# Optimization experiments

Hardware: AMD Instinct MI355X
Metric: run time of the kernel (lower is better)

Reference implementation:

```python
import jax, jax.numpy as jnp
import numpy as np

B, S, HID = 2, 2048, 2048
N_HEADS, N_KV = 16, 8
HEAD_DIM = HID // N_HEADS  # 128
N_REP = N_HEADS // N_KV


def setup_inputs() -> dict:
    key = jax.random.key(0)
    ks = jax.random.split(key, 5)
    x = jax.random.normal(ks[0], (B, S, HID), dtype=jnp.float32)
    Wq = jax.random.normal(ks[1], (HID, N_HEADS * HEAD_DIM), dtype=jnp.float32) * 0.02
    Wk = jax.random.normal(ks[2], (HID, N_KV * HEAD_DIM), dtype=jnp.float32) * 0.02
    Wv = jax.random.normal(ks[3], (HID, N_KV * HEAD_DIM), dtype=jnp.float32) * 0.02
    Wo = jax.random.normal(ks[4], (N_HEADS * HEAD_DIM, HID), dtype=jnp.float32) * 0.02
    # standard RoPE frequencies: theta_i = 10000^(-2i/head_dim), angle = pos * theta_i
    inv_freq = 1.0 / (10000.0 ** (jnp.arange(0, HEAD_DIM, 2, dtype=jnp.float32) / HEAD_DIM))
    angles = jnp.arange(S, dtype=jnp.float32)[:, None] * inv_freq[None, :]  # [S, HEAD_DIM/2]
    return {
        "x": x, "Wq": Wq, "Wk": Wk, "Wv": Wv, "Wo": Wo,
        "freqs_cos": jnp.cos(angles), "freqs_sin": jnp.sin(angles),
        "start_pos": 0,
    }


def _rope(t, cos, sin):
    # t: [B, S, h, head_dim]; complex-view pairs are (even, odd) along last dim
    tr = t.reshape(*t.shape[:-1], -1, 2)
    re, im = tr[..., 0], tr[..., 1]
    cos = cos[None, :, None, :]
    sin = sin[None, :, None, :]
    out_re = re * cos - im * sin
    out_im = re * sin + im * cos
    return jnp.stack([out_re, out_im], axis=-1).reshape(t.shape)


def reference(x, Wq, Wk, Wv, Wo, freqs_cos, freqs_sin, start_pos):
    b, s, _ = x.shape
    xq = (x @ Wq).reshape(b, s, N_HEADS, HEAD_DIM)
    xk = (x @ Wk).reshape(b, s, N_KV, HEAD_DIM)
    xv = (x @ Wv).reshape(b, s, N_KV, HEAD_DIM)
    xq = _rope(xq, freqs_cos, freqs_sin)
    xk = _rope(xk, freqs_cos, freqs_sin)
    # repeat_kv: each kv head duplicated n_rep times consecutively
    xk = jnp.repeat(xk, N_REP, axis=2)  # [b, s, N_HEADS, hd]
    xv = jnp.repeat(xv, N_REP, axis=2)
    scale = 1.0 / jnp.sqrt(jnp.float32(HEAD_DIM))
    attn = jnp.einsum("bqhd,bkhd->bhqk", xq, xk) * scale
    attn = jax.nn.softmax(attn, axis=-1)
    out = jnp.einsum("bhqk,bkhd->bqhd", attn, xv).reshape(b, s, N_HEADS * HEAD_DIM)
    return out @ Wo
```

## Files before the change

kernel.cpp:

```cpp
#include <hip/hip_runtime.h>
#include <stdint.h>

#define DI __device__ __forceinline__

typedef unsigned short u16;
typedef unsigned int   u32;
typedef __attribute__((ext_vector_type(8))) short short8;
typedef __attribute__((ext_vector_type(4))) float f32x4;


DI u16 f2bf(float f) {
    u32 u = __float_as_uint(f);
    u32 r = u + 0x7fff + ((u >> 16) & 1);
    return (u16)(r >> 16);
}
DI u32 pk2bf(float a, float b) {
    return (u32)f2bf(a) | ((u32)f2bf(b) << 16);
}
DI float bf2f(u16 h) { return __uint_as_float(((u32)h) << 16); }

DI f32x4 mfma16(short8 a, short8 b, f32x4 c) {
    return __builtin_amdgcn_mfma_f32_16x16x32_bf16(a, b, c, 0, 0, 0);
}

DI void gload_lds16(const void* g, void* l) {
    __builtin_amdgcn_global_load_lds(
        (const __attribute__((address_space(1))) void*)g,
        (__attribute__((address_space(3))) void*)l, 16, 0, 0);
}

__global__ __launch_bounds__(256) void cvt_x(const float* __restrict__ x,
                                             u16* __restrict__ o, int n4) {
    int i = blockIdx.x * 256 + threadIdx.x;
    if (i >= n4) return;
    float4 v = *(const float4*)(x + (size_t)i * 4);
    uint2 p; p.x = pk2bf(v.x, v.y); p.y = pk2bf(v.z, v.w);
    *(uint2*)(o + (size_t)i * 4) = p;
}

__global__ __launch_bounds__(256) void transpose_cvt(const float* __restrict__ W,
                                                     u16* __restrict__ WT,
                                                     int K, int N) {
    __shared__ u16 tl[64][65];
    int tx = threadIdx.x & 15, ty = threadIdx.x >> 4;
    int tc = blockIdx.x * 64, tr = blockIdx.y * 64;
#pragma unroll
    for (int i = 0; i < 4; i++) {
        int r = tr + ty + i * 16;
        float4 v = *(const float4*)&W[(size_t)r * N + tc + tx * 4];
        tl[tx*4+0][ty+i*16] = f2bf(v.x);
        tl[tx*4+1][ty+i*16] = f2bf(v.y);
        tl[tx*4+2][ty+i*16] = f2bf(v.z);
        tl[tx*4+3][ty+i*16] = f2bf(v.w);
    }
    __syncthreads();
#pragma unroll
    for (int i = 0; i < 4; i++) {
        int n = tc + ty + i * 16;
        uint2 p;
        p.x = (u32)tl[ty+i*16][tx*4+0] | ((u32)tl[ty+i*16][tx*4+1] << 16);
        p.y = (u32)tl[ty+i*16][tx*4+2] | ((u32)tl[ty+i*16][tx*4+3] << 16);
        *(uint2*)&WT[(size_t)n * K + tr + tx * 4] = p;
    }
}

__global__ __launch_bounds__(256) void rope_kernel(u16* __restrict__ buf,
                                                   const float* __restrict__ fc,
                                                   const float* __restrict__ fs,
                                                   int H, int tokshift, int total,
                                                   float oscale) {
    int idx = blockIdx.x * 256 + threadIdx.x;
    if (idx >= total) return;
    int tok = idx >> tokshift;
    int rem = idx & ((1 << tokshift) - 1);
    int h = rem >> 6, j = rem & 63;
    int s = tok & 2047;
    size_t a = ((size_t)tok * H + h) * 128 + 2 * j;
    u32 v = *(u32*)(buf + a);
    float re = bf2f((u16)(v & 0xffff));
    float im = bf2f((u16)(v >> 16));
    float c = fc[s * 64 + j], sn = fs[s * 64 + j];
    *(u32*)(buf + a) = pk2bf((re * c - im * sn) * oscale,
                             (re * sn + im * c) * oscale);
}

__global__ __launch_bounds__(512) void gemm_qkv8(const u16* __restrict__ A,
                                                 const u16* __restrict__ BT,
                                                 u16* __restrict__ Qo,
                                                 u16* __restrict__ Ko,
                                                 u16* __restrict__ Vo) {
    __shared__ __align__(16) u16 SM[65536];
    char* smb = (char*)SM;
    const int tid = threadIdx.x;
    const int w = tid >> 6, l = tid & 63;
    const int l15 = l & 15, lh = l >> 4;
    const int wr = w >> 2, wc = w & 3;

    const int bid = blockIdx.x;
    const int sw = (bid & 7) * 32 + (bid >> 3);
    const int bx = sw & 15, by = sw >> 4;

    const char* Ag = (const char*)A  + (size_t)(by * 256) * 4096;
    const char* Bg = (const char*)BT + (size_t)(bx * 256) * 4096;

    const int r0 = tid >> 3;
    const int c0 = ((tid & 7) << 4) ^ (((tid >> 5) & 1) << 5);
    const int wb = w << 10;

#define STG_A(tt, bb, hh) do {                                              \
        const char* s_ = Ag + (size_t)((hh) * 128 + r0) * 4096 + (tt) * 128 + c0; \
        char* d_ = smb + (bb) * 65536 + (hh) * 16384 + wb;                  \
        gload_lds16(s_, d_);                                                \
        gload_lds16(s_ + (size_t)64 * 4096, d_ + 8192);                     \
    } while (0)
#define STG_B(tt, bb, hh) do {                                              \
        const char* s_ = Bg + (size_t)((hh) * 128 + r0) * 4096 + (tt) * 128 + c0; \
        char* d_ = smb + (bb) * 65536 + 32768 + (hh) * 16384 + wb;          \
        gload_lds16(s_, d_);                                                \
        gload_lds16(s_ + (size_t)64 * 4096, d_ + 8192);                     \
    } while (0)

    const int aoff = l15 * 128 + ((lh * 16) ^ (((l15 >> 2) & 1) << 5));

    const f32x4 fz = {0.f, 0.f, 0.f, 0.f};
    f32x4 acc[8][4];
#pragma unroll
    for (int m = 0; m < 8; m++)
#pragma unroll
        for (int n = 0; n < 4; n++) acc[m][n] = fz;

    STG_A(0, 0, 0); STG_A(0, 0, 1); STG_B(0, 0, 0); STG_B(0, 0, 1);
    STG_A(1, 1, 0);
    asm volatile("s_waitcnt vmcnt(2)" ::: "memory");
    __builtin_amdgcn_s_barrier();

    for (int t = 0; t < 32; ++t) {
        const int cur = t & 1;
        const int t1 = t + 1 < 32 ? t + 1 : 31;
        const int t2 = t + 2 < 32 ? t + 2 : 31;
        const char* Ab = smb + cur * 65536 + wr * 16384 + aoff;
        const char* Bb = smb + cur * 65536 + 32768 + (wc >> 1) * 16384
                         + (wc & 1) * 8192 + aoff;
        short8 aF[4][2], bF[4][2];

        STG_A(t1, cur ^ 1, 1);
#pragma unroll
        for (int m = 0; m < 4; m++) {
            aF[m][0] = *(const short8*)(Ab + m * 2048);
            aF[m][1] = *(const short8*)(Ab + m * 2048 + 64);
        }
#pragma unroll
        for (int n = 0; n < 2; n++) {
            bF[n][0] = *(const short8*)(Bb + n * 2048);
            bF[n][1] = *(const short8*)(Bb + n * 2048 + 64);
        }
        __builtin_amdgcn_s_setprio(1);
#pragma unroll
        for (int m = 0; m < 4; m++)
#pragma unroll
            for (int n = 0; n < 2; n++) {
                acc[m][n] = mfma16(aF[m][0], bF[n][0], acc[m][n]);
                acc[m][n] = mfma16(aF[m][1], bF[n][1], acc[m][n]);
            }
        __builtin_amdgcn_s_setprio(0);
        __builtin_amdgcn_s_barrier();

        STG_B(t1, cur ^ 1, 0);
#pragma unroll
        for (int n = 2; n < 4; n++) {
            bF[n][0] = *(const short8*)(Bb + n * 2048);
            bF[n][1] = *(const short8*)(Bb + n * 2048 + 64);
        }
        __builtin_amdgcn_s_setprio(1);
#pragma unroll
        for (int m = 0; m < 4; m++)
#pragma unroll
            for (int n = 2; n < 4; n++) {
                acc[m][n] = mfma16(aF[m][0], bF[n][0], acc[m][n]);
                acc[m][n] = mfma16(aF[m][1], bF[n][1], acc[m][n]);
            }
        __builtin_amdgcn_s_setprio(0);
        __builtin_amdgcn_s_barrier();

        STG_B(t1, cur ^ 1, 1);
#pragma unroll
        for (int m = 0; m < 4; m++) {
            aF[m][0] = *(const short8*)(Ab + (m + 4) * 2048);
            aF[m][1] = *(const short8*)(Ab + (m + 4) * 2048 + 64);
        }
        __builtin_amdgcn_s_setprio(1);
#pragma unroll
        for (int m = 0; m < 4; m++)
#pragma unroll
            for (int n = 0; n < 2; n++) {
                acc[m + 4][n] = mfma16(aF[m][0], bF[n][0], acc[m + 4][n]);
                acc[m + 4][n] = mfma16(aF[m][1], bF[n][1], acc[m + 4][n]);
            }
        __builtin_amdgcn_s_setprio(0);
        __builtin_amdgcn_s_barrier();

        STG_A(t2, cur, 0);
        __builtin_amdgcn_s_setprio(1);
#pragma unroll
        for (int m = 0; m < 4; m++)
#pragma unroll
            for (int n = 2; n < 4; n++) {
                acc[m + 4][n] = mfma16(aF[m][0], bF[n][0], acc[m + 4][n]);
                acc[m + 4][n] = mfma16(aF[m][1], bF[n][1], acc[m + 4][n]);
            }
        __builtin_amdgcn_s_setprio(0);
        asm volatile("s_waitcnt vmcnt(2)" ::: "memory");
        __builtin_amdgcn_s_barrier();
    }
#undef STG_A
#undef STG_B

    const int rbase = by * 256 + wr * 128 + lh * 4;
    const int cbase = bx * 256 + wc * 64 + l15;
    if (bx < 8) {
#pragma unroll
        for (int m = 0; m < 8; m++)
#pragma unroll
            for (int j = 0; j < 4; j++) {
                size_t ro = (size_t)(rbase + m * 16 + j) * 2048 + cbase;
#pragma unroll
                for (int n = 0; n < 4; n++)
                    Qo[ro + n * 16] = f2bf(acc[m][n][j]);
            }
    } else if (bx < 12) {
        const int ck = cbase - 2048;
#pragma unroll
        for (int m = 0; m < 8; m++)
#pragma unroll
            for (int j = 0; j < 4; j++) {
                size_t ro = (size_t)(rbase + m * 16 + j) * 1024 + ck;
#pragma unroll
                for (int n = 0; n < 4; n++)
                    Ko[ro + n * 16] = f2bf(acc[m][n][j]);
            }
    } else {
#pragma unroll
        for (int m = 0; m < 8; m++)
#pragma unroll
            for (int n = 0; n < 4; n++) {
                int tok = rbase + m * 16;
                int c = cbase + n * 16 - 3072;
                int bb2 = tok >> 11, ss = tok & 2047;
                int h2 = c >> 7, d = c & 127;
                uint2 v;
                v.x = pk2bf(acc[m][n][0], acc[m][n][1]);
                v.y = pk2bf(acc[m][n][2], acc[m][n][3]);
                *(uint2*)(Vo + (size_t)((bb2 * 8 + h2) * 128 + d) * 2048 + ss) = v;
            }
    }
}

__global__ __launch_bounds__(256) void gemm_wo(const u16* __restrict__ A,
                                               const u16* __restrict__ BT,
                                               float* __restrict__ Of,
                                               int M, int N, int K) {
    __shared__ u16 As[128 * 32];
    __shared__ u16 Bs[128 * 32];
    const int tid = threadIdx.x;
    const int w = tid >> 6, l = tid & 63;
    const int m0 = blockIdx.y * 128, n0 = blockIdx.x * 128;
    const int wr = w >> 1, wc = w & 1;
    const int l15 = l & 15, lh = l >> 4;

    const f32x4 fz = {0.f, 0.f, 0.f, 0.f};
    f32x4 acc[4][4];
#pragma unroll
    for (int m = 0; m < 4; m++)
#pragma unroll
        for (int n = 0; n < 4; n++) acc[m][n] = fz;

    const int rowA = w * 32 + (l >> 2);
    const int colb = (l & 3) * 8;

    for (int k0 = 0; k0 < K; k0 += 32) {
        __syncthreads();
#pragma unroll
        for (int c = 0; c < 2; c++) {
            gload_lds16(A  + (size_t)(m0 + rowA + c * 16) * K + k0 + colb,
                        &As[w * 1024 + c * 512]);
            gload_lds16(BT + (size_t)(n0 + rowA + c * 16) * K + k0 + colb,
                        &Bs[w * 1024 + c * 512]);
        }
        __syncthreads();
        short8 af[4], bfr[4];
#pragma unroll
        for (int m = 0; m < 4; m++)
            af[m] = *(const short8*)&As[(wr * 64 + m * 16 + l15) * 32 + lh * 8];
#pragma unroll
        for (int n = 0; n < 4; n++)
            bfr[n] = *(const short8*)&Bs[(wc * 64 + n * 16 + l15) * 32 + lh * 8];
#pragma unroll
        for (int m = 0; m < 4; m++)
#pragma unroll
            for (int n = 0; n < 4; n++)
                acc[m][n] = mfma16(af[m], bfr[n], acc[m][n]);
    }

    const int rbase = m0 + wr * 64 + lh * 4;
    const int cbase = n0 + wc * 64 + l15;
#pragma unroll
    for (int m = 0; m < 4; m++)
#pragma unroll
        for (int j = 0; j < 4; j++) {
            size_t ro = (size_t)(rbase + m * 16 + j) * N + cbase;
#pragma unroll
            for (int n = 0; n < 4; n++)
                Of[ro + n * 16] = acc[m][n][j];
        }
}

__global__ __launch_bounds__(512, 4) void attn_kernel(const u16* __restrict__ Q,
                                                      const u16* __restrict__ Kg,
                                                      const u16* __restrict__ Vg,
                                                      u16* __restrict__ O) {
    __shared__ __align__(16) u16 Ks[2][8192];
    __shared__ __align__(16) u16 Vs[2][8192];
    __shared__ __align__(16) u16 Ps[8][1024];
    const int tid = threadIdx.x;
    const int w = tid >> 6, l = tid & 63;
    const int qt = blockIdx.x, bh = blockIdx.y;
    const int b = bh >> 4, h = bh & 15, h2 = h >> 1;
    const int l15 = l & 15, lh = l >> 4;

    char* KsB = (char*)&Ks[0][0];
    char* VsB = (char*)&Vs[0][0];
    char* PsB = (char*)&Ps[w][0];

    const char* Kbase = (const char*)Kg + (size_t)b * 2048 * 2048 + h2 * 256;
    const char* Vbase = (const char*)Vg + (size_t)(b * 8 + h2) * 128 * 4096;
    const int X0 = tid * 16, X1 = 8192 + tid * 16;
    const int kr0 = X0 >> 8, kc0 = (X0 & 255) ^ ((kr0 & 7) << 4);
    const int kr1 = X1 >> 8, kc1 = (X1 & 255) ^ ((kr1 & 7) << 4);
    const int vd0 = X0 >> 7, vc0 = (X0 & 127) ^ ((vd0 & 7) << 4);
    const int vd1 = X1 >> 7, vc1 = (X1 & 127) ^ ((vd1 & 7) << 4);
    const int wb = w << 10;

#define STAGE(t, pb) do {                                              \
        const char* Kt = Kbase + (size_t)(t) * 131072;                 \
        const char* Vt = Vbase + (t) * 128;                            \
        char* kd = KsB + (pb) * 16384;                                 \
        char* vd = VsB + (pb) * 16384;                                 \
        gload_lds16(Kt + kr0 * 2048 + kc0, kd + wb);                   \
        gload_lds16(Kt + kr1 * 2048 + kc1, kd + 8192 + wb);            \
        gload_lds16(Vt + vd0 * 4096 + vc0, vd + wb);                   \
        gload_lds16(Vt + vd1 * 4096 + vc1, vd + 8192 + wb);            \
    } while (0)

    short8 qf[4];
    {
        const u16* qp = Q + ((size_t)(b * 2048 + qt * 128 + w * 16 + l15)) * 2048
                          + h * 128 + lh * 8;
#pragma unroll
        for (int ks = 0; ks < 4; ks++) qf[ks] = *(const short8*)(qp + ks * 32);
    }

    const f32x4 fz = {0.f, 0.f, 0.f, 0.f};
    f32x4 o[8];
#pragma unroll
    for (int n = 0; n < 8; n++) o[n] = fz;
    float mrow[4] = {-1e30f, -1e30f, -1e30f, -1e30f};
    float lsum[4] = {0.f, 0.f, 0.f, 0.f};

    STAGE(0, 0);

    for (int t = 0; t < 32; t++) {
        __syncthreads();
        const int pb = t & 1;
        if (t < 31) STAGE(t + 1, pb ^ 1);
        const char* kc = KsB + pb * 16384;
        const char* vc = VsB + pb * 16384;
        const int swz = (l15 & 7) << 4;

        f32x4 s[4];
#pragma unroll
        for (int ct = 0; ct < 4; ct++) {
            s[ct] = fz;
#pragma unroll
            for (int ks = 0; ks < 4; ks++) {
                short8 kf = *(const short8*)(kc + ((ct * 16 + l15) << 8)
                                                + ((ks * 64 + lh * 16) ^ swz));
                s[ct] = mfma16(qf[ks], kf, s[ct]);
            }
        }

        float pl[4];
#pragma unroll
        for (int r = 0; r < 4; r++)
            pl[r] = fmaxf(fmaxf(s[0][r], s[1][r]), fmaxf(s[2][r], s[3][r]));
        bool grow = (pl[0] > mrow[0] + 8.f) || (pl[1] > mrow[1] + 8.f) ||
                    (pl[2] > mrow[2] + 8.f) || (pl[3] > mrow[3] + 8.f);
        if (__any(grow)) {
#pragma unroll
            for (int r = 0; r < 4; r++) {
                float mx = pl[r];
                mx = fmaxf(mx, __shfl_xor(mx, 1));
                mx = fmaxf(mx, __shfl_xor(mx, 2));
                mx = fmaxf(mx, __shfl_xor(mx, 4));
                mx = fmaxf(mx, __shfl_xor(mx, 8));
                float mnew = fmaxf(mrow[r], mx);
                float fsc = exp2f(mrow[r] - mnew);
                mrow[r] = mnew;
                lsum[r] *= fsc;
#pragma unroll
                for (int n = 0; n < 8; n++) o[n][r] *= fsc;
            }
        }
#pragma unroll
        for (int r = 0; r < 4; r++) {
            float p0 = exp2f(s[0][r] - mrow[r]);
            float p1 = exp2f(s[1][r] - mrow[r]);
            float p2 = exp2f(s[2][r] - mrow[r]);
            float p3 = exp2f(s[3][r] - mrow[r]);
            lsum[r] += (p0 + p1) + (p2 + p3);
            const int rw = lh * 4 + r;
            const int rb = rw << 7;
            const int sw2 = (rw & 7) << 4;
            const int cb2 = l15 << 1;
            *(u16*)(PsB + (rb + (( 0 + cb2) ^ sw2))) =
                (u16)((__float_as_uint(p0) + 0x8000u) >> 16);
            *(u16*)(PsB + (rb + ((32 + cb2) ^ sw2))) =
                (u16)((__float_as_uint(p1) + 0x8000u) >> 16);
            *(u16*)(PsB + (rb + ((64 + cb2) ^ sw2))) =
                (u16)((__float_as_uint(p2) + 0x8000u) >> 16);
            *(u16*)(PsB + (rb + ((96 + cb2) ^ sw2))) =
                (u16)((__float_as_uint(p3) + 0x8000u) >> 16);
        }

#pragma unroll
        for (int ks2 = 0; ks2 < 2; ks2++) {
            short8 pf = *(const short8*)(PsB + ((l15 << 7)
                                + ((ks2 * 64 + lh * 16) ^ swz)));
#pragma unroll
            for (int n = 0; n < 8; n++) {
                short8 vf = *(const short8*)(vc + (((n * 16 + l15) << 7)
                                                  + ((ks2 * 64 + lh * 16) ^ swz)));
                o[n] = mfma16(pf, vf, o[n]);
            }
        }
    }

    const size_t ob = ((size_t)(b * 2048 + qt * 128 + w * 16 + lh * 4)) * 2048
                      + h * 128 + l15;
#pragma unroll
    for (int r = 0; r < 4; r++) {
        float ls = lsum[r];
        ls += __shfl_xor(ls, 1);
        ls += __shfl_xor(ls, 2);
        ls += __shfl_xor(ls, 4);
        ls += __shfl_xor(ls, 8);
        float li = 1.0f / ls;
#pragma unroll
        for (int n = 0; n < 8; n++)
            O[ob + (size_t)r * 2048 + n * 16] = f2bf(o[n][r] * li);
    }
#undef STAGE
}

extern "C" void kernel_launch(void* const* d_in, const int* in_sizes, int n_in,
                              void* d_out, int out_size, void* d_ws, size_t ws_size,
                              hipStream_t stream) {
    const float* x  = (const float*)d_in[0];
    const float* Wq = (const float*)d_in[1];
    const float* Wk = (const float*)d_in[2];
    const float* Wv = (const float*)d_in[3];
    const float* Wo = (const float*)d_in[4];
    const float* fc = (const float*)d_in[5];
    const float* fs = (const float*)d_in[6];
    float* out = (float*)d_out;

    uint8_t* ws = (uint8_t*)d_ws;
    u16* xb   = (u16*)(ws + 0);
    u16* wqkv = (u16*)(ws + 16777216);
    u16* wqT  = (u16*)(ws + 16777216);
    u16* wkT  = (u16*)(ws + 25165824);
    u16* wvT  = (u16*)(ws + 29360128);
    u16* woT  = (u16*)(ws + 33554432);
    u16* qb   = (u16*)(ws + 41943040);
    u16* kb   = (u16*)(ws + 58720256);
    u16* vT   = (u16*)(ws + 67108864);
    u16* ao   = xb;

    cvt_x<<<dim3(8192), dim3(256), 0, stream>>>(x, xb, 2097152);
    transpose_cvt<<<dim3(32, 32), dim3(256), 0, stream>>>(Wq, wqT, 2048, 2048);
    transpose_cvt<<<dim3(16, 32), dim3(256), 0, stream>>>(Wk, wkT, 2048, 1024);
    transpose_cvt<<<dim3(16, 32), dim3(256), 0, stream>>>(Wv, wvT, 2048, 1024);
    transpose_cvt<<<dim3(32, 32), dim3(256), 0, stream>>>(Wo, woT, 2048, 2048);

    gemm_qkv8<<<dim3(256), dim3(512), 0, stream>>>(xb, wqkv, qb, kb, vT);

    rope_kernel<<<dim3(16384), dim3(256), 0, stream>>>(qb, fc, fs, 16, 10, 4194304,
                                                       0.12751742987f);
    rope_kernel<<<dim3(8192),  dim3(256), 0, stream>>>(kb, fc, fs, 8, 9, 2097152, 1.0f);

    attn_kernel<<<dim3(16, 32), dim3(512), 0, stream>>>(qb, kb, vT, ao);

    gemm_wo<<<dim3(16, 32), dim3(256), 0, stream>>>(ao, woT, out, 4096, 2048, 2048);
}
```

Baseline: 265.3 us.

## Give each attention wave two query tiles and merge weight transposes into one launch

The attention kernel now runs 4 waves of 256 threads per block instead of 8. Each wave handles 32 query rows as two 16-row tiles, so every K and V fragment read from LDS feeds two MFMAs. That halves LDS fragment traffic per FLOP, at the cost of doubled accumulator registers and lower occupancy (launch bounds 256,2). Separately, the four weight transpose-convert launches are merged into one 3D-grid launch, with early exit for the narrower K and V matrices, to cut launch overhead.

```diff
diff --git a/kernel.cpp b/kernel.cpp
--- a/kernel.cpp
+++ b/kernel.cpp
@@ -38,9 +38,23 @@
     *(uint2*)(o + (size_t)i * 4) = p;
 }
 
-__global__ __launch_bounds__(256) void transpose_cvt(const float* __restrict__ W,
-                                                     u16* __restrict__ WT,
-                                                     int K, int N) {
+__global__ __launch_bounds__(256) void transpose_cvt4(const float* __restrict__ W0,
+                                                      const float* __restrict__ W1,
+                                                      const float* __restrict__ W2,
+                                                      const float* __restrict__ W3,
+                                                      u16* __restrict__ D0,
+                                                      u16* __restrict__ D1,
+                                                      u16* __restrict__ D2,
+                                                      u16* __restrict__ D3) {
+    const float* W; u16* D; int N;
+    switch (blockIdx.z) {
+        case 0:  W = W0; D = D0; N = 2048; break;
+        case 1:  W = W1; D = D1; N = 1024; break;
+        case 2:  W = W2; D = D2; N = 1024; break;
+        default: W = W3; D = D3; N = 2048; break;
+    }
+    if ((int)blockIdx.x >= (N >> 6)) return;
+    const int K = 2048;
     __shared__ u16 tl[64][65];
     int tx = threadIdx.x & 15, ty = threadIdx.x >> 4;
     int tc = blockIdx.x * 64, tr = blockIdx.y * 64;
@@ -60,7 +74,7 @@
         uint2 p;
         p.x = (u32)tl[ty+i*16][tx*4+0] | ((u32)tl[ty+i*16][tx*4+1] << 16);
         p.y = (u32)tl[ty+i*16][tx*4+2] | ((u32)tl[ty+i*16][tx*4+3] << 16);
-        *(uint2*)&WT[(size_t)n * K + tr + tx * 4] = p;
+        *(uint2*)&D[(size_t)n * K + tr + tx * 4] = p;
     }
 }
 
@@ -314,13 +328,13 @@
         }
 }
 
-__global__ __launch_bounds__(512, 4) void attn_kernel(const u16* __restrict__ Q,
+__global__ __launch_bounds__(256, 2) void attn_kernel(const u16* __restrict__ Q,
                                                       const u16* __restrict__ Kg,
                                                       const u16* __restrict__ Vg,
                                                       u16* __restrict__ O) {
     __shared__ __align__(16) u16 Ks[2][8192];
     __shared__ __align__(16) u16 Vs[2][8192];
-    __shared__ __align__(16) u16 Ps[8][1024];
+    __shared__ __align__(16) u16 Ps[4][2048];
     const int tid = threadIdx.x;
     const int w = tid >> 6, l = tid & 63;
     const int qt = blockIdx.x, bh = blockIdx.y;
@@ -333,38 +347,45 @@
 
     const char* Kbase = (const char*)Kg + (size_t)b * 2048 * 2048 + h2 * 256;
     const char* Vbase = (const char*)Vg + (size_t)(b * 8 + h2) * 128 * 4096;
-    const int X0 = tid * 16, X1 = 8192 + tid * 16;
-    const int kr0 = X0 >> 8, kc0 = (X0 & 255) ^ ((kr0 & 7) << 4);
-    const int kr1 = X1 >> 8, kc1 = (X1 & 255) ^ ((kr1 & 7) << 4);
-    const int vd0 = X0 >> 7, vc0 = (X0 & 127) ^ ((vd0 & 7) << 4);
-    const int vd1 = X1 >> 7, vc1 = (X1 & 127) ^ ((vd1 & 7) << 4);
-    const int wb = w << 10;
-
-#define STAGE(t, pb) do {                                              \
-        const char* Kt = Kbase + (size_t)(t) * 131072;                 \
-        const char* Vt = Vbase + (t) * 128;                            \
-        char* kd = KsB + (pb) * 16384;                                 \
-        char* vd = VsB + (pb) * 16384;                                 \
-        gload_lds16(Kt + kr0 * 2048 + kc0, kd + wb);                   \
-        gload_lds16(Kt + kr1 * 2048 + kc1, kd + 8192 + wb);            \
-        gload_lds16(Vt + vd0 * 4096 + vc0, vd + wb);                   \
-        gload_lds16(Vt + vd1 * 4096 + vc1, vd + 8192 + wb);            \
+    int krow[4], kcol[4], vrow[4], vcol[4];
+#pragma unroll
+    for (int c = 0; c < 4; c++) {
+        int X = c * 4096 + tid * 16;
+        krow[c] = X >> 8; kcol[c] = (X & 255) ^ ((krow[c] & 7) << 4);
+        vrow[c] = X >> 7; vcol[c] = (X & 127) ^ ((vrow[c] & 7) << 4);
+    }
+
+#define STAGE(t, pb) do {                                               \
+        const char* Kt = Kbase + (size_t)(t) * 131072;                  \
+        const char* Vt = Vbase + (t) * 128;                             \
+        char* kd = KsB + (pb) * 16384 + tid * 16;                       \
+        char* vd = VsB + (pb) * 16384 + tid * 16;                       \
+        _Pragma("unroll")                                               \
+        for (int c = 0; c < 4; c++) {                                   \
+            gload_lds16(Kt + krow[c] * 2048 + kcol[c], kd + c * 4096);  \
+            gload_lds16(Vt + (size_t)vrow[c] * 4096 + vcol[c], vd + c * 4096); \
+        }                                                               \
     } while (0)
 
-    short8 qf[4];
+    short8 qf0[4], qf1[4];
     {
-        const u16* qp = Q + ((size_t)(b * 2048 + qt * 128 + w * 16 + l15)) * 2048
+        const u16* qp = Q + ((size_t)(b * 2048 + qt * 128 + w * 32 + l15)) * 2048
                           + h * 128 + lh * 8;
 #pragma unroll
-        for (int ks = 0; ks < 4; ks++) qf[ks] = *(const short8*)(qp + ks * 32);
+        for (int ks = 0; ks < 4; ks++) {
+            qf0[ks] = *(const short8*)(qp + ks * 32);
+            qf1[ks] = *(const short8*)(qp + 16 * 2048 + ks * 32);
+        }
     }
 
     const f32x4 fz = {0.f, 0.f, 0.f, 0.f};
-    f32x4 o[8];
-#pragma unroll
-    for (int n = 0; n < 8; n++) o[n] = fz;
-    float mrow[4] = {-1e30f, -1e30f, -1e30f, -1e30f};
-    float lsum[4] = {0.f, 0.f, 0.f, 0.f};
+    f32x4 o0[8], o1[8];
+#pragma unroll
+    for (int n = 0; n < 8; n++) { o0[n] = fz; o1[n] = fz; }
+    float mrow0[4] = {-1e30f, -1e30f, -1e30f, -1e30f};
+    float mrow1[4] = {-1e30f, -1e30f, -1e30f, -1e30f};
+    float lsum0[4] = {0.f, 0.f, 0.f, 0.f};
+    float lsum1[4] = {0.f, 0.f, 0.f, 0.f};
 
     STAGE(0, 0);
 
@@ -376,51 +397,70 @@
         const char* vc = VsB + pb * 16384;
         const int swz = (l15 & 7) << 4;
 
-        f32x4 s[4];
+        f32x4 s0[4], s1[4];
 #pragma unroll
         for (int ct = 0; ct < 4; ct++) {
-            s[ct] = fz;
+            s0[ct] = fz; s1[ct] = fz;
 #pragma unroll
             for (int ks = 0; ks < 4; ks++) {
                 short8 kf = *(const short8*)(kc + ((ct * 16 + l15) << 8)
                                                 + ((ks * 64 + lh * 16) ^ swz));
-                s[ct] = mfma16(qf[ks], kf, s[ct]);
-            }
-        }
-
-        float pl[4];
+                s0[ct] = mfma16(qf0[ks], kf, s0[ct]);
+                s1[ct] = mfma16(qf1[ks], kf, s1[ct]);
+            }
+        }
+
+        float pl0[4], pl1[4];
+#pragma unroll
+        for (int r = 0; r < 4; r++) {
+            pl0[r] = fmaxf(fmaxf(s0[0][r], s0[1][r]), fmaxf(s0[2][r], s0[3][r]));
+            pl1[r] = fmaxf(fmaxf(s1[0][r], s1[1][r]), fmaxf(s1[2][r], s1[3][r]));
+        }
+        bool grow = false;
 #pragma unroll
         for (int r = 0; r < 4; r++)
-            pl[r] = fmaxf(fmaxf(s[0][r], s[1][r]), fmaxf(s[2][r], s[3][r]));
-        bool grow = (pl[0] > mrow[0] + 8.f) || (pl[1] > mrow[1] + 8.f) ||
-                    (pl[2] > mrow[2] + 8.f) || (pl[3] > mrow[3] + 8.f);
+            grow = grow || (pl0[r] > mrow0[r] + 8.f) || (pl1[r] > mrow1[r] + 8.f);
         if (__any(grow)) {
 #pragma unroll
             for (int r = 0; r < 4; r++) {
-                float mx = pl[r];
+                float mx = pl0[r];
                 mx = fmaxf(mx, __shfl_xor(mx, 1));
                 mx = fmaxf(mx, __shfl_xor(mx, 2));
                 mx = fmaxf(mx, __shfl_xor(mx, 4));
                 mx = fmaxf(mx, __shfl_xor(mx, 8));
-                float mnew = fmaxf(mrow[r], mx);
-                float fsc = exp2f(mrow[r] - mnew);
-                mrow[r] = mnew;
-                lsum[r] *= fsc;
-#pragma unroll
-                for (int n = 0; n < 8; n++) o[n][r] *= fsc;
-            }
-        }
+                float mnew = fmaxf(mrow0[r], mx);
+                float fsc = exp2f(mrow0[r] - mnew);
+                mrow0[r] = mnew;
+                lsum0[r] *= fsc;
+#pragma unroll
+                for (int n = 0; n < 8; n++) o0[n][r] *= fsc;
+            }
+#pragma unroll
+            for (int r = 0; r < 4; r++) {
+                float mx = pl1[r];
+                mx = fmaxf(mx, __shfl_xor(mx, 1));
+                mx = fmaxf(mx, __shfl_xor(mx, 2));
+                mx = fmaxf(mx, __shfl_xor(mx, 4));
+                mx = fmaxf(mx, __shfl_xor(mx, 8));
+                float mnew = fmaxf(mrow1[r], mx);
+                float fsc = exp2f(mrow1[r] - mnew);
+                mrow1[r] = mnew;
+                lsum1[r] *= fsc;
+#pragma unroll
+                for (int n = 0; n < 8; n++) o1[n][r] *= fsc;
+            }
+        }
+        const int cb2 = l15 << 1;
 #pragma unroll
         for (int r = 0; r < 4; r++) {
-            float p0 = exp2f(s[0][r] - mrow[r]);
-            float p1 = exp2f(s[1][r] - mrow[r]);
-            float p2 = exp2f(s[2][r] - mrow[r]);
-            float p3 = exp2f(s[3][r] - mrow[r]);
-            lsum[r] += (p0 + p1) + (p2 + p3);
+            float p0 = exp2f(s0[0][r] - mrow0[r]);
+            float p1 = exp2f(s0[1][r] - mrow0[r]);
+            float p2 = exp2f(s0[2][r] - mrow0[r]);
+            float p3 = exp2f(s0[3][r] - mrow0[r]);
+            lsum0[r] += (p0 + p1) + (p2 + p3);
             const int rw = lh * 4 + r;
             const int rb = rw << 7;
             const int sw2 = (rw & 7) << 4;
-            const int cb2 = l15 << 1;
             *(u16*)(PsB + (rb + (( 0 + cb2) ^ sw2))) =
                 (u16)((__float_as_uint(p0) + 0x8000u) >> 16);
             *(u16*)(PsB + (rb + ((32 + cb2) ^ sw2))) =
@@ -430,25 +470,47 @@
             *(u16*)(PsB + (rb + ((96 + cb2) ^ sw2))) =
                 (u16)((__float_as_uint(p3) + 0x8000u) >> 16);
         }
+#pragma unroll
+        for (int r = 0; r < 4; r++) {
+            float p0 = exp2f(s1[0][r] - mrow1[r]);
+            float p1 = exp2f(s1[1][r] - mrow1[r]);
+            float p2 = exp2f(s1[2][r] - mrow1[r]);
+            float p3 = exp2f(s1[3][r] - mrow1[r]);
+            lsum1[r] += (p0 + p1) + (p2 + p3);
+            const int rw = 16 + lh * 4 + r;
+            const int rb = rw << 7;
+            const int sw2 = (rw & 7) << 4;
+            *(u16*)(PsB + (rb + (( 0 + cb2) ^ sw2))) =
+                (u16)((__float_as_uint(p0) + 0x8000u) >> 16);
+            *(u16*)(PsB + (rb + ((32 + cb2) ^ sw2))) =
+                (u16)((__float_as_uint(p1) + 0x8000u) >> 16);
+            *(u16*)(PsB + (rb + ((64 + cb2) ^ sw2))) =
+                (u16)((__float_as_uint(p2) + 0x8000u) >> 16);
+            *(u16*)(PsB + (rb + ((96 + cb2) ^ sw2))) =
+                (u16)((__float_as_uint(p3) + 0x8000u) >> 16);
+        }
 
 #pragma unroll
         for (int ks2 = 0; ks2 < 2; ks2++) {
-            short8 pf = *(const short8*)(PsB + ((l15 << 7)
+            short8 pf0 = *(const short8*)(PsB + ((l15 << 7)
+                                + ((ks2 * 64 + lh * 16) ^ swz)));
+            short8 pf1 = *(const short8*)(PsB + (((16 + l15) << 7)
                                 + ((ks2 * 64 + lh * 16) ^ swz)));
 #pragma unroll
             for (int n = 0; n < 8; n++) {
                 short8 vf = *(const short8*)(vc + (((n * 16 + l15) << 7)
                                                   + ((ks2 * 64 + lh * 16) ^ swz)));
-                o[n] = mfma16(pf, vf, o[n]);
-            }
-        }
-    }
-
-    const size_t ob = ((size_t)(b * 2048 + qt * 128 + w * 16 + lh * 4)) * 2048
-                      + h * 128 + l15;
+                o0[n] = mfma16(pf0, vf, o0[n]);
+                o1[n] = mfma16(pf1, vf, o1[n]);
+            }
+        }
+    }
+
+    const size_t ob0 = ((size_t)(b * 2048 + qt * 128 + w * 32 + lh * 4)) * 2048
+                       + h * 128 + l15;
 #pragma unroll
     for (int r = 0; r < 4; r++) {
-        float ls = lsum[r];
+        float ls = lsum0[r];
         ls += __shfl_xor(ls, 1);
         ls += __shfl_xor(ls, 2);
         ls += __shfl_xor(ls, 4);
@@ -456,7 +518,20 @@
         float li = 1.0f / ls;
 #pragma unroll
         for (int n = 0; n < 8; n++)
-            O[ob + (size_t)r * 2048 + n * 16] = f2bf(o[n][r] * li);
+            O[ob0 + (size_t)r * 2048 + n * 16] = f2bf(o0[n][r] * li);
+    }
+    const size_t ob1 = ob0 + (size_t)16 * 2048;
+#pragma unroll
+    for (int r = 0; r < 4; r++) {
+        float ls = lsum1[r];
+        ls += __shfl_xor(ls, 1);
+        ls += __shfl_xor(ls, 2);
+        ls += __shfl_xor(ls, 4);
+        ls += __shfl_xor(ls, 8);
+        float li = 1.0f / ls;
+#pragma unroll
+        for (int n = 0; n < 8; n++)
+            O[ob1 + (size_t)r * 2048 + n * 16] = f2bf(o1[n][r] * li);
     }
 #undef STAGE
 }
@@ -486,10 +561,8 @@
     u16* ao   = xb;
 
     cvt_x<<<dim3(8192), dim3(256), 0, stream>>>(x, xb, 2097152);
-    transpose_cvt<<<dim3(32, 32), dim3(256), 0, stream>>>(Wq, wqT, 2048, 2048);
-    transpose_cvt<<<dim3(16, 32), dim3(256), 0, stream>>>(Wk, wkT, 2048, 1024);
-    transpose_cvt<<<dim3(16, 32), dim3(256), 0, stream>>>(Wv, wvT, 2048, 1024);
-    transpose_cvt<<<dim3(32, 32), dim3(256), 0, stream>>>(Wo, woT, 2048, 2048);
+    transpose_cvt4<<<dim3(32, 32, 4), dim3(256), 0, stream>>>(Wq, Wk, Wv, Wo,
+                                                              wqT, wkT, wvT, woT);
 
     gemm_qkv8<<<dim3(256), dim3(512), 0, stream>>>(xb, wqkv, qb, kb, vT);
 
@@ -497,7 +570,7 @@
                                                        0.12751742987f);
     rope_kernel<<<dim3(8192),  dim3(256), 0, stream>>>(kb, fc, fs, 8, 9, 2097152, 1.0f);
 
-    attn_kernel<<<dim3(16, 32), dim3(512), 0, stream>>>(qb, kb, vT, ao);
+    attn_kernel<<<dim3(16, 32), dim3(256), 0, stream>>>(qb, kb, vT, ao);
 
     gemm_wo<<<dim3(16, 32), dim3(256), 0, stream>>>(ao, woT, out, 4096, 2048, 2048);
 }
```

After: 256.0 us. -3.5%, faster.
